# Kernel tuning notes

Hardware: AMD Instinct MI355X
Metric: run time of the kernel (lower is better)

## Reference

```python
import jax, jax.numpy as jnp
import numpy as np

B, C, H, W, KS = 8, 3, 512, 512, 3
K = KS * KS  # kernel_elements = 9


def setup_inputs() -> dict:
    key = jax.random.key(0)
    ks = jax.random.split(key, 5)
    return {
        "x": jax.random.normal(ks[0], (B, C, H, W), jnp.float32),
        "w1": jax.random.normal(ks[1], (K - 1, C, KS, KS), jnp.float32) * 0.1,  # find_ref conv weight
        "b1": jax.random.normal(ks[2], (K - 1,), jnp.float32) * 0.1,
        "w2": jax.random.normal(ks[3], (C, K), jnp.float32) * 0.1,  # grouped 1x1 conv: C groups, K in-ch each
        "b2": jax.random.normal(ks[4], (C,), jnp.float32) * 0.1,
    }


def _grid_sample_bilinear(img_nhwc, gx, gy):
    # torch.grid_sample, mode='bilinear', padding_mode='zeros', align_corners=False
    # img_nhwc: [B,H,W,C]; gx,gy: [B,h,w,K] normalized coords (x=width, y=height)
    Bs, Hh, Ww, _ = img_nhwc.shape
    ix = ((gx + 1.0) * Ww - 1.0) * 0.5
    iy = ((gy + 1.0) * Hh - 1.0) * 0.5
    ix0 = jnp.floor(ix)
    iy0 = jnp.floor(iy)
    wx1 = ix - ix0
    wy1 = iy - iy0
    wx0 = 1.0 - wx1
    wy0 = 1.0 - wy1
    bidx = jnp.arange(Bs)[:, None, None, None]

    def corner(yc, xc, wgt):
        valid = (xc >= 0) & (xc < Ww) & (yc >= 0) & (yc < Hh)
        xi = jnp.clip(xc, 0, Ww - 1).astype(jnp.int32)
        yi = jnp.clip(yc, 0, Hh - 1).astype(jnp.int32)
        v = img_nhwc[bidx, yi, xi]  # [B,h,w,K,C]
        return v * (wgt * valid)[..., None]

    out = corner(iy0, ix0, wy0 * wx0)
    out = out + corner(iy0, ix0 + 1.0, wy0 * wx1)
    out = out + corner(iy0 + 1.0, ix0, wy1 * wx0)
    out = out + corner(iy0 + 1.0, ix0 + 1.0, wy1 * wx1)
    return out  # [B,h,w,K,C]


def _forward(x, w1, b1, w2, b2):
    Bs, Cc, Hh, Ww = x.shape
    pad = KS // 2
    # find_ref: conv3x3 (pad=1) + sigmoid -> offsets in [0,1]
    off = jax.lax.conv_general_dilated(
        x, w1, (1, 1), ((pad, pad), (pad, pad)),
        dimension_numbers=("NCHW", "OIHW", "NCHW"))
    off = jax.nn.sigmoid(off + b1[None, :, None, None])  # [B,K-1,H,W]
    off = jnp.transpose(off, (0, 2, 3, 1)).reshape(Bs, Hh, Ww, (K - 1) // 2, 2)
    ctr = float(KS // 2)
    sym = 2.0 * ctr - off  # find_symmetric_points
    center = jnp.zeros((Bs, Hh, Ww, 1, 2), off.dtype)
    off_all = jnp.concatenate([off, center, sym], axis=-2)  # [B,H,W,K,2]
    # base grid: stack(h_grid, w_grid) with linspace(0,1)
    base = jnp.stack(
        jnp.meshgrid(jnp.linspace(0.0, 1.0, Hh), jnp.linspace(0.0, 1.0, Ww), indexing="ij"),
        axis=-1)  # [H,W,2]
    coords = base[None, :, :, None, :] + off_all  # [B,H,W,K,2]
    # grid_sample interprets last dim as (x=width, y=height)
    gx = coords[..., 0]
    gy = coords[..., 1]
    img = jnp.transpose(x, (0, 2, 3, 1))  # [B,H,W,C]
    sampled = _grid_sample_bilinear(img, gx, gy)  # [B,H,W,K,C]
    # concatenation order in torch: elem-major channels -> [B, K*C, H, W]
    deformed = jnp.transpose(sampled, (0, 3, 4, 1, 2)).reshape(Bs, K * Cc, Hh, Ww)
    # grouped 1x1 conv: groups=C, group g consumes channels [g*K:(g+1)*K]
    grp = deformed.reshape(Bs, Cc, K, Hh, Ww)
    out = jnp.einsum("bgkhw,gk->bghw", grp, w2) + b2[None, :, None, None]
    return jax.nn.relu(out)


def reference(x, w1, b1, w2, b2):
    return _forward(x, w1, b1, w2, b2)
```

## Files before the change

### kernel.cpp

```cpp
#include <hip/hip_runtime.h>

#define BATCH 8
#define HDIM  512
#define WDIM  512
#define PLANE (HDIM * WDIM)

#define QC_N      129
#define YROW0     254
#define YROWS     259
#define YSTRIDE   260
#define QSTRIDE   (YSTRIDE * 16)
#define PARSTRIDE (QC_N * QSTRIDE)
#define IMGSTRIDE (2 * PARSTRIDE)

typedef _Float16 half2v __attribute__((ext_vector_type(2)));
typedef _Float16 half8v __attribute__((ext_vector_type(8)));
typedef float    f2v    __attribute__((ext_vector_type(2)));

struct __align__(16) HQuad { half2v p0, p1, p2, p3; };

#if __has_builtin(__builtin_amdgcn_fdot2)
#define FDOT2(a, b, c) __builtin_amdgcn_fdot2((a), (b), (c), false)
#else
#define FDOT2(a, b, c) fmaf((float)(a).x, (float)(b).x, fmaf((float)(a).y, (float)(b).y, (c)))
#endif

#if __has_builtin(__builtin_amdgcn_exp2f)
#define EXP2F(x) __builtin_amdgcn_exp2f(x)
#else
#define EXP2F(x) exp2f(x)
#endif

__global__ __launch_bounds__(256) void repack_tiles(
    const float* __restrict__ x,
    char* __restrict__ xp)
{
    int b    = blockIdx.x & 7;
    int rest = blockIdx.x >> 3;
    int p    = rest & 1;
    int Qc   = rest >> 1;
    int xb0  = 254 + 2 * Qc + p;
    int x1   = xb0 + 1;
    bool x1v = (x1 < 512);

    const float* xb = x + (size_t)b * 3 * PLANE;
    char* dst = xp + (size_t)b * IMGSTRIDE + (size_t)p * PARSTRIDE
                   + (size_t)Qc * QSTRIDE;

    for (int t = threadIdx.x; t < YROWS; t += 256) {
        int y = YROW0 + t;
        half8v o;
        if (y < 512) {
            int base = (y << 9) + xb0;
            float a0 = xb[base];
            float a1 = xb[PLANE + base];
            float a2 = xb[2 * PLANE + base];
            float b0 = 0.f, b1c = 0.f, b2c = 0.f;
            if (x1v) {
                b0  = xb[base + 1];
                b1c = xb[PLANE + base + 1];
                b2c = xb[2 * PLANE + base + 1];
            }
            o[0] = (_Float16)a0; o[1] = (_Float16)a1; o[2] = (_Float16)a2; o[3] = (_Float16)0.f;
            o[4] = (_Float16)b0; o[5] = (_Float16)b1c; o[6] = (_Float16)b2c; o[7] = (_Float16)0.f;
        } else {
#pragma unroll
            for (int k = 0; k < 8; k++) o[k] = (_Float16)0.f;
        }
        *(half8v*)(dst + (size_t)t * 16) = o;
    }
}

__global__ __launch_bounds__(256) void seesaw_v11(
    const float* __restrict__ x,
    const char* __restrict__ xpack,
    const float* __restrict__ w1, const float* __restrict__ b1,
    const float* __restrict__ w2, const float* __restrict__ b2,
    float* __restrict__ out)
{
    int t  = threadIdx.x;
    int b  = blockIdx.x & 7;
    int i  = blockIdx.x >> 3;
    int j0 = t << 1;

    const float* xb = x + (size_t)b * 3 * PLANE;
    const char*  hb = xpack + (size_t)b * IMGSTRIDE;

    int cm = j0 - 1; if (cm < 0) cm = 0;
    int cp = j0 + 2; if (cp > 511) cp = 511;
    bool jlo = (t == 0), jhi = (t == 255);

    float vm[9], va[9], vb9[9], vp9[9];
    if (i >= 1 && i <= 510) {
#pragma unroll
        for (int di = 0; di < 3; di++) {
            const float* row = xb + ((i + di - 1) << 9);
#pragma unroll
            for (int c = 0; c < 3; c++) {
                const float* rc = row + c * PLANE;
                float m = rc[cm]; if (jlo) m = 0.f;
                f2v  mid = *(const f2v*)(rc + j0);
                float pv = rc[cp]; if (jhi) pv = 0.f;
                int r = c * 3 + di;
                vm[r] = m; va[r] = mid[0]; vb9[r] = mid[1]; vp9[r] = pv;
            }
        }
    } else {
#pragma unroll
        for (int di = 0; di < 3; di++) {
            int y = i + di - 1;
            bool yv = (unsigned)y < (unsigned)HDIM;
            const float* row = xb + ((yv ? y : 0) << 9);
#pragma unroll
            for (int c = 0; c < 3; c++) {
                const float* rc = row + c * PLANE;
                float m = rc[cm]; if (jlo || !yv) m = 0.f;
                f2v  mid = *(const f2v*)(rc + j0);
                float pv = rc[cp]; if (jhi || !yv) pv = 0.f;
                float m0 = yv ? mid[0] : 0.f;
                float m1 = yv ? mid[1] : 0.f;
                int r = c * 3 + di;
                vm[r] = m; va[r] = m0; vb9[r] = m1; vp9[r] = pv;
            }
        }
    }
    __builtin_amdgcn_sched_barrier(0);

    float tap0[27], tap1[27];
#pragma unroll
    for (int c = 0; c < 3; c++)
#pragma unroll
        for (int di = 0; di < 3; di++) {
            int r = c * 3 + di, k = c * 9 + di * 3;
            tap0[k]     = vm[r];  tap0[k + 1] = va[r];  tap0[k + 2] = vb9[r];
            tap1[k]     = va[r];  tap1[k + 1] = vb9[r]; tap1[k + 2] = vp9[r];
        }

    const float NLOG2E = -1.44269504f;
    auto conv8 = [&](const float* tap, float* s2) {
        f2v V[13];
#pragma unroll
        for (int k = 0; k < 13; k++) { V[k][0] = tap[2 * k]; V[k][1] = tap[2 * k + 1]; }
#pragma unroll
        for (int e = 0; e < 8; e++) {
            const float* we = w1 + e * 27;
            f2v a2; a2[0] = b1[e]; a2[1] = 0.f;
#pragma unroll
            for (int k = 0; k < 13; k++) {
                f2v ww; ww[0] = we[2 * k]; ww[1] = we[2 * k + 1];
                a2 = __builtin_elementwise_fma(V[k], ww, a2);
            }
            float acc = a2[0] + a2[1] + tap[26] * we[26];
            s2[e] = 256.0f * __builtin_amdgcn_rcpf(1.0f + EXP2F(acc * NLOG2E));
        }
    };
    float s0[8], s1[8];
    conv8(tap0, s0);
    conv8(tap1, s1);

    half2v w2a[5], w2b[5];
#pragma unroll
    for (int q = 0; q < 5; q++) {
        w2a[q][0] = (_Float16)w2[q * 3];
        w2a[q][1] = (_Float16)w2[q * 3 + 1];
        w2b[q][0] = (_Float16)w2[q * 3 + 2];
        w2b[q][1] = (_Float16)0.f;
    }

    const float k511 = 256.0f / 511.0f;
    float fxb = fmaf((float)i, k511, 255.5f);
    float fy0 = fmaf((float)j0, k511, 255.5f);
    float fy1 = fy0 + k511;

    int   adrA[5], adrB[5];
    float wXA[5][2], wYA[5][2], wXB[5][2], wYB[5][2];
    auto phase1 = [&](const float* s2, float fyb, int (&adr)[5],
                      float (&wX)[5][2], float (&wY)[5][2]) {
#pragma unroll
        for (int q = 0; q < 5; q++) {
            float ixf = (q < 4) ? (fxb + s2[2 * q])     : fxb;
            float iyf = (q < 4) ? (fyb + s2[2 * q + 1]) : fyb;
            int ix0 = (int)ixf, iy0 = (int)iyf;
            float wx1 = ixf - (float)ix0, wy1 = iyf - (float)iy0;
            wX[q][0] = (ix0 <= 511) ? (1.f - wx1) : 0.f;
            wX[q][1] = (ix0 <= 510) ? wx1 : 0.f;
            wY[q][0] = (iy0 <= 511) ? (1.f - wy1) : 0.f;
            wY[q][1] = (iy0 <= 510) ? wy1 : 0.f;
            int x0c = min(ix0, 511);
            int y0c = min(iy0, 511);
            int Qc  = (x0c >> 1) - 127;
            int off = (Qc << 12) + (Qc << 6) + ((y0c - 254) << 4);
            adr[q] = off + ((x0c & 1) ? PARSTRIDE : 0);
        }
    };

    phase1(s0, fy0, adrA, wXA, wYA);
    HQuad qA[5][2];
#pragma unroll
    for (int q = 0; q < 5; q++) {
        qA[q][0] = *(const HQuad*)(hb + (size_t)adrA[q]);
        qA[q][1] = *(const HQuad*)(hb + (size_t)adrA[q] + 16);
    }
    phase1(s1, fy1, adrB, wXB, wYB);
    HQuad qB[5][2];
#pragma unroll
    for (int q = 0; q < 5; q++) {
        qB[q][0] = *(const HQuad*)(hb + (size_t)adrB[q]);
        qB[q][1] = *(const HQuad*)(hb + (size_t)adrB[q] + 16);
    }
    __builtin_amdgcn_sched_barrier(0);

    float ogA[3] = {0.f, 0.f, 0.f}, ogB[3] = {0.f, 0.f, 0.f};
    auto phase3 = [&](HQuad (&qv)[5][2], float (&wX)[5][2], float (&wY)[5][2], float* og) {
#pragma unroll
        for (int q = 0; q < 5; q++) {
            int g = q / 3;
            float dl0 = FDOT2(qv[q][0].p0, w2a[q], FDOT2(qv[q][0].p1, w2b[q], 0.f));
            float dh0 = FDOT2(qv[q][0].p2, w2a[q], FDOT2(qv[q][0].p3, w2b[q], 0.f));
            float dl1 = FDOT2(qv[q][1].p0, w2a[q], FDOT2(qv[q][1].p1, w2b[q], 0.f));
            float dh1 = FDOT2(qv[q][1].p2, w2a[q], FDOT2(qv[q][1].p3, w2b[q], 0.f));
            float r0 = fmaf(dh0, wX[q][1], dl0 * wX[q][0]);
            float r1 = fmaf(dh1, wX[q][1], dl1 * wX[q][0]);
            og[g] = fmaf(r1, wY[q][1], fmaf(r0, wY[q][0], og[g]));
        }
    };
    phase3(qA, wXA, wYA, ogA);
    phase3(qB, wXB, wYB, ogB);

    if ((i | j0) == 0) {
#pragma unroll
        for (int p = 5; p < 9; p++) {
            float ixf = fxb + 512.0f - s0[2 * (p - 5)];
            float iyf = fy0 + 512.0f - s0[2 * (p - 5) + 1];
            float ix0f = floorf(ixf), iy0f = floorf(iyf);
            float wx1 = ixf - ix0f, wy1 = iyf - iy0f;
            float wx0 = 1.f - wx1,  wy0 = 1.f - wy1;
            int ix0 = (int)ix0f, iy0 = (int)iy0f;
            float t0 = 0.f, t1 = 0.f, t2 = 0.f;
            for (int cy = 0; cy < 2; cy++) {
                int yc2 = iy0 + cy;
                if (yc2 < 0 || yc2 >= HDIM) continue;
                float wy = cy ? wy1 : wy0;
                for (int cx = 0; cx < 2; cx++) {
                    int xcc2 = ix0 + cx;
                    if (xcc2 < 0 || xcc2 >= WDIM) continue;
                    float wgt = wy * (cx ? wx1 : wx0);
                    int base = (yc2 << 9) + xcc2;
                    t0 = fmaf(xb[base],             wgt, t0);
                    t1 = fmaf(xb[PLANE + base],     wgt, t1);
                    t2 = fmaf(xb[2 * PLANE + base], wgt, t2);
                }
            }
            int g  = p / 3;
            int k0 = (p % 3) * 3;
            ogA[g] = fmaf(t0, w2[g * 9 + k0 + 0], ogA[g]);
            ogA[g] = fmaf(t1, w2[g * 9 + k0 + 1], ogA[g]);
            ogA[g] = fmaf(t2, w2[g * 9 + k0 + 2], ogA[g]);
        }
    }

    size_t ob = (size_t)(b * 3) * PLANE + ((size_t)i << 9) + j0;
#pragma unroll
    for (int g = 0; g < 3; g++) {
        float u0 = ogA[g] + b2[g];
        float u1 = ogB[g] + b2[g];
        f2v st;
        st[0] = u0 > 0.f ? u0 : 0.f;
        st[1] = u1 > 0.f ? u1 : 0.f;
        *(f2v*)(out + ob + (size_t)g * PLANE) = st;
    }
}

__global__ __launch_bounds__(256) void seesaw_fused_v1(
    const float* __restrict__ x, const float* __restrict__ w1,
    const float* __restrict__ b1, const float* __restrict__ w2,
    const float* __restrict__ b2, float* __restrict__ out)
{
    int t = threadIdx.x;
    int gid = blockIdx.x * 256 + t;
    int j = gid & (WDIM - 1);
    int i = (gid >> 9) & (HDIM - 1);
    int b = gid >> 18;
    const float* xb = x + (size_t)b * 3 * PLANE;
    float acc[8];
#pragma unroll
    for (int e = 0; e < 8; e++) acc[e] = b1[e];
#pragma unroll
    for (int di = 0; di < 3; di++) {
        int y = i + di - 1;
        if (y < 0 || y >= HDIM) continue;
#pragma unroll
        for (int dj = 0; dj < 3; dj++) {
            int xc = j + dj - 1;
            if (xc < 0 || xc >= WDIM) continue;
            size_t base = (size_t)y * WDIM + xc;
#pragma unroll
            for (int c = 0; c < 3; c++) {
                float v = xb[(size_t)c * PLANE + base];
#pragma unroll
                for (int e = 0; e < 8; e++)
                    acc[e] = fmaf(v, w1[e * 27 + c * 9 + di * 3 + dj], acc[e]);
            }
        }
    }
    float s[8];
#pragma unroll
    for (int e = 0; e < 8; e++) s[e] = 1.0f / (1.0f + __expf(-acc[e]));
    const float inv511 = 1.0f / 511.0f;
    float bx = (float)i * inv511, by = (float)j * inv511;
    float og0 = 0.f, og1 = 0.f, og2 = 0.f;
#pragma unroll
    for (int p = 0; p < 9; p++) {
        float c0, c1;
        if (p < 4)       { c0 = s[2 * p];              c1 = s[2 * p + 1]; }
        else if (p == 4) { c0 = 0.f;                   c1 = 0.f; }
        else             { c0 = 2.0f - s[2 * (p - 5)]; c1 = 2.0f - s[2 * (p - 5) + 1]; }
        float ixf = (bx + c0) * 256.0f + 255.5f;
        float iyf = (by + c1) * 256.0f + 255.5f;
        float ix0f = floorf(ixf), iy0f = floorf(iyf);
        float wx1 = ixf - ix0f, wy1 = iyf - iy0f;
        float wx0 = 1.f - wx1,  wy0 = 1.f - wy1;
        int ix0 = (int)ix0f, iy0 = (int)iy0f;
        float s0 = 0.f, s1 = 0.f, s2 = 0.f;
#pragma unroll
        for (int cy = 0; cy < 2; cy++) {
            int yc = iy0 + cy;
            if (yc < 0 || yc >= HDIM) continue;
            float wy = cy ? wy1 : wy0;
#pragma unroll
            for (int cx = 0; cx < 2; cx++) {
                int xcc = ix0 + cx;
                if (xcc < 0 || xcc >= WDIM) continue;
                float wgt = wy * (cx ? wx1 : wx0);
                size_t base = (size_t)yc * WDIM + xcc;
                s0 = fmaf(xb[base],             wgt, s0);
                s1 = fmaf(xb[PLANE + base],     wgt, s1);
                s2 = fmaf(xb[2 * PLANE + base], wgt, s2);
            }
        }
        int g  = p / 3;
        int k0 = (p % 3) * 3;
        float* og = (g == 0) ? &og0 : (g == 1) ? &og1 : &og2;
        *og = fmaf(s0, w2[g * 9 + k0 + 0], *og);
        *og = fmaf(s1, w2[g * 9 + k0 + 1], *og);
        *og = fmaf(s2, w2[g * 9 + k0 + 2], *og);
    }
    size_t ob = (size_t)(b * 3) * PLANE + (size_t)i * WDIM + j;
    float v0 = og0 + b2[0], v1 = og1 + b2[1], v2 = og2 + b2[2];
    out[ob]             = v0 > 0.f ? v0 : 0.f;
    out[ob + PLANE]     = v1 > 0.f ? v1 : 0.f;
    out[ob + 2 * PLANE] = v2 > 0.f ? v2 : 0.f;
}

extern "C" void kernel_launch(void* const* d_in, const int* in_sizes, int n_in,
                              void* d_out, int out_size, void* d_ws, size_t ws_size,
                              hipStream_t stream) {
    const float* x  = (const float*)d_in[0];
    const float* w1 = (const float*)d_in[1];
    const float* b1 = (const float*)d_in[2];
    const float* w2 = (const float*)d_in[3];
    const float* b2 = (const float*)d_in[4];
    float* out = (float*)d_out;

    int total = BATCH * HDIM * WDIM;
    size_t need = (size_t)BATCH * IMGSTRIDE + 16;

    if (ws_size >= need) {
        repack_tiles<<<8 * 2 * QC_N, 256, 0, stream>>>(x, (char*)d_ws);
        seesaw_v11<<<BATCH * HDIM, 256, 0, stream>>>(x, (const char*)d_ws,
                                                     w1, b1, w2, b2, out);
    } else {
        seesaw_fused_v1<<<total / 256, 256, 0, stream>>>(x, w1, b1, w2, b2, out);
    }
}
```

Before: 131.9 us.

## Precompute per-tap channel dot products in repack with 2x2 corner quads

The repack kernel now folds the grouped 1x1 conv weights into the image ahead of time. It stores, for each of the five sampled taps, the fp16 dot product over channels for every 2x2 corner neighbourhood, laid out by x/y parity so that one 8-byte load returns all four bilinear corners. The main kernel then does 5 small loads per pixel instead of 10 16-byte loads and drops the fdot2 work. The cost is a larger workspace (five planes of quads) and a repack that reads each input four times. The old v11 path remains as a fallback when the workspace is too small.

```diff
diff --git a/kernel.cpp b/kernel.cpp
--- a/kernel.cpp
+++ b/kernel.cpp
@@ -4,6 +4,11 @@
 #define HDIM  512
 #define WDIM  512
 #define PLANE (HDIM * WDIM)
+
+#define QN      129
+#define QPAIRS  (QN * QN)
+#define QPLANE  (4 * QPAIRS * 8)
+#define IMG12   (5 * QPLANE)
 
 #define QC_N      129
 #define YROW0     254
@@ -14,10 +19,12 @@
 #define IMGSTRIDE (2 * PARSTRIDE)
 
 typedef _Float16 half2v __attribute__((ext_vector_type(2)));
+typedef _Float16 half4v __attribute__((ext_vector_type(4)));
 typedef _Float16 half8v __attribute__((ext_vector_type(8)));
 typedef float    f2v    __attribute__((ext_vector_type(2)));
 
 struct __align__(16) HQuad { half2v p0, p1, p2, p3; };
+struct __align__(8)  HPair { half2v lo, hi; };
 
 #if __has_builtin(__builtin_amdgcn_fdot2)
 #define FDOT2(a, b, c) __builtin_amdgcn_fdot2((a), (b), (c), false)
@@ -31,47 +38,52 @@
 #define EXP2F(x) exp2f(x)
 #endif
 
-__global__ __launch_bounds__(256) void repack_tiles(
+__global__ __launch_bounds__(256) void repack_dots(
     const float* __restrict__ x,
+    const float* __restrict__ w2,
     char* __restrict__ xp)
 {
-    int b    = blockIdx.x & 7;
-    int rest = blockIdx.x >> 3;
-    int p    = rest & 1;
-    int Qc   = rest >> 1;
-    int xb0  = 254 + 2 * Qc + p;
-    int x1   = xb0 + 1;
-    bool x1v = (x1 < 512);
+    int b  = blockIdx.x & 7;
+    int P  = (blockIdx.x >> 3) & 3;
+    int Qy = blockIdx.x >> 5;
+    int Qx = threadIdx.x;
+    if (Qx >= QN) return;
+    int px = P & 1, py = P >> 1;
+    int X0 = 2 * Qx + 254 + px;
+    int Y0 = 2 * Qy + 254 + py;
 
     const float* xb = x + (size_t)b * 3 * PLANE;
-    char* dst = xp + (size_t)b * IMGSTRIDE + (size_t)p * PARSTRIDE
-                   + (size_t)Qc * QSTRIDE;
-
-    for (int t = threadIdx.x; t < YROWS; t += 256) {
-        int y = YROW0 + t;
-        half8v o;
-        if (y < 512) {
-            int base = (y << 9) + xb0;
-            float a0 = xb[base];
-            float a1 = xb[PLANE + base];
-            float a2 = xb[2 * PLANE + base];
-            float b0 = 0.f, b1c = 0.f, b2c = 0.f;
-            if (x1v) {
-                b0  = xb[base + 1];
-                b1c = xb[PLANE + base + 1];
-                b2c = xb[2 * PLANE + base + 1];
-            }
-            o[0] = (_Float16)a0; o[1] = (_Float16)a1; o[2] = (_Float16)a2; o[3] = (_Float16)0.f;
-            o[4] = (_Float16)b0; o[5] = (_Float16)b1c; o[6] = (_Float16)b2c; o[7] = (_Float16)0.f;
-        } else {
-#pragma unroll
-            for (int k = 0; k < 8; k++) o[k] = (_Float16)0.f;
-        }
-        *(half8v*)(dst + (size_t)t * 16) = o;
+
+    float vc[4][3];
+#pragma unroll
+    for (int cy = 0; cy < 2; cy++)
+#pragma unroll
+        for (int cx = 0; cx < 2; cx++) {
+            int xx = X0 + cx, yy = Y0 + cy;
+            bool vld = (xx <= 511) && (yy <= 511);
+            int xs = min(xx, 511), ys = min(yy, 511);
+            int base = (ys << 9) + xs;
+            int ci = cy * 2 + cx;
+            vc[ci][0] = vld ? xb[base]             : 0.f;
+            vc[ci][1] = vld ? xb[PLANE + base]     : 0.f;
+            vc[ci][2] = vld ? xb[2 * PLANE + base] : 0.f;
+        }
+
+    char* dst = xp + (size_t)b * IMG12 + (size_t)((P * QPAIRS + Qy * QN + Qx) << 3);
+#pragma unroll
+    for (int q = 0; q < 5; q++) {
+        float wa = w2[3 * q], wb = w2[3 * q + 1], wc = w2[3 * q + 2];
+        half4v o;
+#pragma unroll
+        for (int ci = 0; ci < 4; ci++) {
+            float v = fmaf(vc[ci][2], wc, fmaf(vc[ci][1], wb, vc[ci][0] * wa));
+            o[ci] = (_Float16)v;
+        }
+        *(half4v*)(dst + q * QPLANE) = o;
     }
 }
 
-__global__ __launch_bounds__(256) void seesaw_v11(
+__global__ __launch_bounds__(256) void seesaw_v12(
     const float* __restrict__ x,
     const char* __restrict__ xpack,
     const float* __restrict__ w1, const float* __restrict__ b1,
@@ -84,7 +96,7 @@
     int j0 = t << 1;
 
     const float* xb = x + (size_t)b * 3 * PLANE;
-    const char*  hb = xpack + (size_t)b * IMGSTRIDE;
+    const char*  hb = xpack + (size_t)b * IMG12;
 
     int cm = j0 - 1; if (cm < 0) cm = 0;
     int cp = j0 + 2; if (cp > 511) cp = 511;
@@ -158,15 +170,6 @@
     conv8(tap0, s0);
     conv8(tap1, s1);
 
-    half2v w2a[5], w2b[5];
-#pragma unroll
-    for (int q = 0; q < 5; q++) {
-        w2a[q][0] = (_Float16)w2[q * 3];
-        w2a[q][1] = (_Float16)w2[q * 3 + 1];
-        w2b[q][0] = (_Float16)w2[q * 3 + 2];
-        w2b[q][1] = (_Float16)0.f;
-    }
-
     const float k511 = 256.0f / 511.0f;
     float fxb = fmaf((float)i, k511, 255.5f);
     float fy0 = fmaf((float)j0, k511, 255.5f);
@@ -186,46 +189,40 @@
             wX[q][1] = (ix0 <= 510) ? wx1 : 0.f;
             wY[q][0] = (iy0 <= 511) ? (1.f - wy1) : 0.f;
             wY[q][1] = (iy0 <= 510) ? wy1 : 0.f;
-            int x0c = min(ix0, 511);
-            int y0c = min(iy0, 511);
-            int Qc  = (x0c >> 1) - 127;
-            int off = (Qc << 12) + (Qc << 6) + ((y0c - 254) << 4);
-            adr[q] = off + ((x0c & 1) ? PARSTRIDE : 0);
+            int x0c = min(ix0, 511), y0c = min(iy0, 511);
+            int P  = ((y0c & 1) << 1) | (x0c & 1);
+            int Qx = (x0c >> 1) - 127;
+            int Qy = (y0c >> 1) - 127;
+            adr[q] = (P * QPAIRS + Qy * QN + Qx) << 3;
         }
     };
 
     phase1(s0, fy0, adrA, wXA, wYA);
-    HQuad qA[5][2];
-#pragma unroll
-    for (int q = 0; q < 5; q++) {
-        qA[q][0] = *(const HQuad*)(hb + (size_t)adrA[q]);
-        qA[q][1] = *(const HQuad*)(hb + (size_t)adrA[q] + 16);
-    }
+    HPair pA[5];
+#pragma unroll
+    for (int q = 0; q < 5; q++)
+        pA[q] = *(const HPair*)(hb + (size_t)(q * QPLANE + adrA[q]));
     phase1(s1, fy1, adrB, wXB, wYB);
-    HQuad qB[5][2];
-#pragma unroll
-    for (int q = 0; q < 5; q++) {
-        qB[q][0] = *(const HQuad*)(hb + (size_t)adrB[q]);
-        qB[q][1] = *(const HQuad*)(hb + (size_t)adrB[q] + 16);
-    }
+    HPair pB[5];
+#pragma unroll
+    for (int q = 0; q < 5; q++)
+        pB[q] = *(const HPair*)(hb + (size_t)(q * QPLANE + adrB[q]));
     __builtin_amdgcn_sched_barrier(0);
 
     float ogA[3] = {0.f, 0.f, 0.f}, ogB[3] = {0.f, 0.f, 0.f};
-    auto phase3 = [&](HQuad (&qv)[5][2], float (&wX)[5][2], float (&wY)[5][2], float* og) {
+    auto phase3 = [&](HPair (&pv)[5], float (&wX)[5][2], float (&wY)[5][2], float* og) {
 #pragma unroll
         for (int q = 0; q < 5; q++) {
             int g = q / 3;
-            float dl0 = FDOT2(qv[q][0].p0, w2a[q], FDOT2(qv[q][0].p1, w2b[q], 0.f));
-            float dh0 = FDOT2(qv[q][0].p2, w2a[q], FDOT2(qv[q][0].p3, w2b[q], 0.f));
-            float dl1 = FDOT2(qv[q][1].p0, w2a[q], FDOT2(qv[q][1].p1, w2b[q], 0.f));
-            float dh1 = FDOT2(qv[q][1].p2, w2a[q], FDOT2(qv[q][1].p3, w2b[q], 0.f));
-            float r0 = fmaf(dh0, wX[q][1], dl0 * wX[q][0]);
-            float r1 = fmaf(dh1, wX[q][1], dl1 * wX[q][0]);
+            float v00 = (float)pv[q].lo[0], v01 = (float)pv[q].lo[1];
+            float v10 = (float)pv[q].hi[0], v11c = (float)pv[q].hi[1];
+            float r0 = fmaf(v01,  wX[q][1], v00 * wX[q][0]);
+            float r1 = fmaf(v11c, wX[q][1], v10 * wX[q][0]);
             og[g] = fmaf(r1, wY[q][1], fmaf(r0, wY[q][0], og[g]));
         }
     };
-    phase3(qA, wXA, wYA, ogA);
-    phase3(qB, wXB, wYB, ogB);
+    phase3(pA, wXA, wYA, ogA);
+    phase3(pB, wXB, wYB, ogB);
 
     if ((i | j0) == 0) {
 #pragma unroll
@@ -271,6 +268,244 @@
     }
 }
 
+__global__ __launch_bounds__(256) void repack_tiles(
+    const float* __restrict__ x, char* __restrict__ xp)
+{
+    int b    = blockIdx.x & 7;
+    int rest = blockIdx.x >> 3;
+    int p    = rest & 1;
+    int Qc   = rest >> 1;
+    int xb0  = 254 + 2 * Qc + p;
+    int x1   = xb0 + 1;
+    bool x1v = (x1 < 512);
+
+    const float* xb = x + (size_t)b * 3 * PLANE;
+    char* dst = xp + (size_t)b * IMGSTRIDE + (size_t)p * PARSTRIDE
+                   + (size_t)Qc * QSTRIDE;
+
+    for (int t = threadIdx.x; t < YROWS; t += 256) {
+        int y = YROW0 + t;
+        half8v o;
+        if (y < 512) {
+            int base = (y << 9) + xb0;
+            float a0 = xb[base];
+            float a1 = xb[PLANE + base];
+            float a2 = xb[2 * PLANE + base];
+            float b0 = 0.f, b1c = 0.f, b2c = 0.f;
+            if (x1v) {
+                b0  = xb[base + 1];
+                b1c = xb[PLANE + base + 1];
+                b2c = xb[2 * PLANE + base + 1];
+            }
+            o[0] = (_Float16)a0; o[1] = (_Float16)a1; o[2] = (_Float16)a2; o[3] = (_Float16)0.f;
+            o[4] = (_Float16)b0; o[5] = (_Float16)b1c; o[6] = (_Float16)b2c; o[7] = (_Float16)0.f;
+        } else {
+#pragma unroll
+            for (int k = 0; k < 8; k++) o[k] = (_Float16)0.f;
+        }
+        *(half8v*)(dst + (size_t)t * 16) = o;
+    }
+}
+
+__global__ __launch_bounds__(256) void seesaw_v11(
+    const float* __restrict__ x, const char* __restrict__ xpack,
+    const float* __restrict__ w1, const float* __restrict__ b1,
+    const float* __restrict__ w2, const float* __restrict__ b2,
+    float* __restrict__ out)
+{
+    int t  = threadIdx.x;
+    int b  = blockIdx.x & 7;
+    int i  = blockIdx.x >> 3;
+    int j0 = t << 1;
+
+    const float* xb = x + (size_t)b * 3 * PLANE;
+    const char*  hb = xpack + (size_t)b * IMGSTRIDE;
+
+    int cm = j0 - 1; if (cm < 0) cm = 0;
+    int cp = j0 + 2; if (cp > 511) cp = 511;
+    bool jlo = (t == 0), jhi = (t == 255);
+
+    float vm[9], va[9], vb9[9], vp9[9];
+    if (i >= 1 && i <= 510) {
+#pragma unroll
+        for (int di = 0; di < 3; di++) {
+            const float* row = xb + ((i + di - 1) << 9);
+#pragma unroll
+            for (int c = 0; c < 3; c++) {
+                const float* rc = row + c * PLANE;
+                float m = rc[cm]; if (jlo) m = 0.f;
+                f2v  mid = *(const f2v*)(rc + j0);
+                float pv = rc[cp]; if (jhi) pv = 0.f;
+                int r = c * 3 + di;
+                vm[r] = m; va[r] = mid[0]; vb9[r] = mid[1]; vp9[r] = pv;
+            }
+        }
+    } else {
+#pragma unroll
+        for (int di = 0; di < 3; di++) {
+            int y = i + di - 1;
+            bool yv = (unsigned)y < (unsigned)HDIM;
+            const float* row = xb + ((yv ? y : 0) << 9);
+#pragma unroll
+            for (int c = 0; c < 3; c++) {
+                const float* rc = row + c * PLANE;
+                float m = rc[cm]; if (jlo || !yv) m = 0.f;
+                f2v  mid = *(const f2v*)(rc + j0);
+                float pv = rc[cp]; if (jhi || !yv) pv = 0.f;
+                float m0 = yv ? mid[0] : 0.f;
+                float m1 = yv ? mid[1] : 0.f;
+                int r = c * 3 + di;
+                vm[r] = m; va[r] = m0; vb9[r] = m1; vp9[r] = pv;
+            }
+        }
+    }
+    __builtin_amdgcn_sched_barrier(0);
+
+    float tap0[27], tap1[27];
+#pragma unroll
+    for (int c = 0; c < 3; c++)
+#pragma unroll
+        for (int di = 0; di < 3; di++) {
+            int r = c * 3 + di, k = c * 9 + di * 3;
+            tap0[k]     = vm[r];  tap0[k + 1] = va[r];  tap0[k + 2] = vb9[r];
+            tap1[k]     = va[r];  tap1[k + 1] = vb9[r]; tap1[k + 2] = vp9[r];
+        }
+
+    const float NLOG2E = -1.44269504f;
+    auto conv8 = [&](const float* tap, float* s2) {
+        f2v V[13];
+#pragma unroll
+        for (int k = 0; k < 13; k++) { V[k][0] = tap[2 * k]; V[k][1] = tap[2 * k + 1]; }
+#pragma unroll
+        for (int e = 0; e < 8; e++) {
+            const float* we = w1 + e * 27;
+            f2v a2; a2[0] = b1[e]; a2[1] = 0.f;
+#pragma unroll
+            for (int k = 0; k < 13; k++) {
+                f2v ww; ww[0] = we[2 * k]; ww[1] = we[2 * k + 1];
+                a2 = __builtin_elementwise_fma(V[k], ww, a2);
+            }
+            float acc = a2[0] + a2[1] + tap[26] * we[26];
+            s2[e] = 256.0f * __builtin_amdgcn_rcpf(1.0f + EXP2F(acc * NLOG2E));
+        }
+    };
+    float s0[8], s1[8];
+    conv8(tap0, s0);
+    conv8(tap1, s1);
+
+    half2v w2a[5], w2b[5];
+#pragma unroll
+    for (int q = 0; q < 5; q++) {
+        w2a[q][0] = (_Float16)w2[q * 3];
+        w2a[q][1] = (_Float16)w2[q * 3 + 1];
+        w2b[q][0] = (_Float16)w2[q * 3 + 2];
+        w2b[q][1] = (_Float16)0.f;
+    }
+
+    const float k511 = 256.0f / 511.0f;
+    float fxb = fmaf((float)i, k511, 255.5f);
+    float fy0 = fmaf((float)j0, k511, 255.5f);
+    float fy1 = fy0 + k511;
+
+    int   adrA[5], adrB[5];
+    float wXA[5][2], wYA[5][2], wXB[5][2], wYB[5][2];
+    auto phase1 = [&](const float* s2, float fyb, int (&adr)[5],
+                      float (&wX)[5][2], float (&wY)[5][2]) {
+#pragma unroll
+        for (int q = 0; q < 5; q++) {
+            float ixf = (q < 4) ? (fxb + s2[2 * q])     : fxb;
+            float iyf = (q < 4) ? (fyb + s2[2 * q + 1]) : fyb;
+            int ix0 = (int)ixf, iy0 = (int)iyf;
+            float wx1 = ixf - (float)ix0, wy1 = iyf - (float)iy0;
+            wX[q][0] = (ix0 <= 511) ? (1.f - wx1) : 0.f;
+            wX[q][1] = (ix0 <= 510) ? wx1 : 0.f;
+            wY[q][0] = (iy0 <= 511) ? (1.f - wy1) : 0.f;
+            wY[q][1] = (iy0 <= 510) ? wy1 : 0.f;
+            int x0c = min(ix0, 511);
+            int y0c = min(iy0, 511);
+            int Qc  = (x0c >> 1) - 127;
+            int off = (Qc << 12) + (Qc << 6) + ((y0c - 254) << 4);
+            adr[q] = off + ((x0c & 1) ? PARSTRIDE : 0);
+        }
+    };
+
+    phase1(s0, fy0, adrA, wXA, wYA);
+    HQuad qA[5][2];
+#pragma unroll
+    for (int q = 0; q < 5; q++) {
+        qA[q][0] = *(const HQuad*)(hb + (size_t)adrA[q]);
+        qA[q][1] = *(const HQuad*)(hb + (size_t)adrA[q] + 16);
+    }
+    phase1(s1, fy1, adrB, wXB, wYB);
+    HQuad qB[5][2];
+#pragma unroll
+    for (int q = 0; q < 5; q++) {
+        qB[q][0] = *(const HQuad*)(hb + (size_t)adrB[q]);
+        qB[q][1] = *(const HQuad*)(hb + (size_t)adrB[q] + 16);
+    }
+    __builtin_amdgcn_sched_barrier(0);
+
+    float ogA[3] = {0.f, 0.f, 0.f}, ogB[3] = {0.f, 0.f, 0.f};
+    auto phase3 = [&](HQuad (&qv)[5][2], float (&wX)[5][2], float (&wY)[5][2], float* og) {
+#pragma unroll
+        for (int q = 0; q < 5; q++) {
+            int g = q / 3;
+            float dl0 = FDOT2(qv[q][0].p0, w2a[q], FDOT2(qv[q][0].p1, w2b[q], 0.f));
+            float dh0 = FDOT2(qv[q][0].p2, w2a[q], FDOT2(qv[q][0].p3, w2b[q], 0.f));
+            float dl1 = FDOT2(qv[q][1].p0, w2a[q], FDOT2(qv[q][1].p1, w2b[q], 0.f));
+            float dh1 = FDOT2(qv[q][1].p2, w2a[q], FDOT2(qv[q][1].p3, w2b[q], 0.f));
+            float r0 = fmaf(dh0, wX[q][1], dl0 * wX[q][0]);
+            float r1 = fmaf(dh1, wX[q][1], dl1 * wX[q][0]);
+            og[g] = fmaf(r1, wY[q][1], fmaf(r0, wY[q][0], og[g]));
+        }
+    };
+    phase3(qA, wXA, wYA, ogA);
+    phase3(qB, wXB, wYB, ogB);
+
+    if ((i | j0) == 0) {
+#pragma unroll
+        for (int p = 5; p < 9; p++) {
+            float ixf = fxb + 512.0f - s0[2 * (p - 5)];
+            float iyf = fy0 + 512.0f - s0[2 * (p - 5) + 1];
+            float ix0f = floorf(ixf), iy0f = floorf(iyf);
+            float wx1 = ixf - ix0f, wy1 = iyf - iy0f;
+            float wx0 = 1.f - wx1,  wy0 = 1.f - wy1;
+            int ix0 = (int)ix0f, iy0 = (int)iy0f;
+            float t0 = 0.f, t1 = 0.f, t2 = 0.f;
+            for (int cy = 0; cy < 2; cy++) {
+                int yc2 = iy0 + cy;
+                if (yc2 < 0 || yc2 >= HDIM) continue;
+                float wy = cy ? wy1 : wy0;
+                for (int cx = 0; cx < 2; cx++) {
+                    int xcc2 = ix0 + cx;
+                    if (xcc2 < 0 || xcc2 >= WDIM) continue;
+                    float wgt = wy * (cx ? wx1 : wx0);
+                    int base = (yc2 << 9) + xcc2;
+                    t0 = fmaf(xb[base],             wgt, t0);
+                    t1 = fmaf(xb[PLANE + base],     wgt, t1);
+                    t2 = fmaf(xb[2 * PLANE + base], wgt, t2);
+                }
+            }
+            int g  = p / 3;
+            int k0 = (p % 3) * 3;
+            ogA[g] = fmaf(t0, w2[g * 9 + k0 + 0], ogA[g]);
+            ogA[g] = fmaf(t1, w2[g * 9 + k0 + 1], ogA[g]);
+            ogA[g] = fmaf(t2, w2[g * 9 + k0 + 2], ogA[g]);
+        }
+    }
+
+    size_t ob = (size_t)(b * 3) * PLANE + ((size_t)i << 9) + j0;
+#pragma unroll
+    for (int g = 0; g < 3; g++) {
+        float u0 = ogA[g] + b2[g];
+        float u1 = ogB[g] + b2[g];
+        f2v st;
+        st[0] = u0 > 0.f ? u0 : 0.f;
+        st[1] = u1 > 0.f ? u1 : 0.f;
+        *(f2v*)(out + ob + (size_t)g * PLANE) = st;
+    }
+}
+
 __global__ __launch_bounds__(256) void seesaw_fused_v1(
     const float* __restrict__ x, const float* __restrict__ w1,
     const float* __restrict__ b1, const float* __restrict__ w2,
@@ -363,9 +598,14 @@
     float* out = (float*)d_out;
 
     int total = BATCH * HDIM * WDIM;
-    size_t need = (size_t)BATCH * IMGSTRIDE + 16;
-
-    if (ws_size >= need) {
+    size_t need12 = (size_t)BATCH * IMG12 + 64;
+    size_t need11 = (size_t)BATCH * IMGSTRIDE + 16;
+
+    if (ws_size >= need12) {
+        repack_dots<<<8 * 4 * QN, 256, 0, stream>>>(x, w2, (char*)d_ws);
+        seesaw_v12<<<BATCH * HDIM, 256, 0, stream>>>(x, (const char*)d_ws,
+                                                     w1, b1, w2, b2, out);
+    } else if (ws_size >= need11) {
         repack_tiles<<<8 * 2 * QC_N, 256, 0, stream>>>(x, (char*)d_ws);
         seesaw_v11<<<BATCH * HDIM, 256, 0, stream>>>(x, (const char*)d_ws,
                                                      w1, b1, w2, b2, out);
```

Result: faster. 120.5 us (-8.6%).

## Pre-reduce channels with w2 in repack, use column-major fp16 table, restructure conv

Applied to the files above, without the earlier changes.

The repack kernel now applies the grouped 1x1 weights per sampling point before storing, so each (q, parity, column) entry holds one fp16 scalar instead of three channels. The main kernel then fetches one 8-byte pair per sample instead of two 16-byte quads and skips the fdot2 channel reductions. The repack also writes a transposed copy of w1, so the offset conv can run as a k-outer loop with paired FMAs across output channels. This cuts gather bytes and ALU work, at the cost of scattered 4-byte writes in the repack and extra rounding from storing the w2-weighted sums in fp16.

```diff
diff --git a/kernel.cpp b/kernel.cpp
--- a/kernel.cpp
+++ b/kernel.cpp
@@ -5,25 +5,16 @@
 #define WDIM  512
 #define PLANE (HDIM * WDIM)
 
-#define QC_N      129
-#define YROW0     254
-#define YROWS     259
-#define YSTRIDE   260
-#define QSTRIDE   (YSTRIDE * 16)
-#define PARSTRIDE (QC_N * QSTRIDE)
-#define IMGSTRIDE (2 * PARSTRIDE)
+#define COLB   1040
+#define NCOL   1290
+#define IMG15  ((size_t)NCOL * COLB)
+#define PACK15 ((size_t)BATCH * IMG15)
+#define W1E_FLOATS (27 * 8)
 
 typedef _Float16 half2v __attribute__((ext_vector_type(2)));
-typedef _Float16 half8v __attribute__((ext_vector_type(8)));
 typedef float    f2v    __attribute__((ext_vector_type(2)));
 
-struct __align__(16) HQuad { half2v p0, p1, p2, p3; };
-
-#if __has_builtin(__builtin_amdgcn_fdot2)
-#define FDOT2(a, b, c) __builtin_amdgcn_fdot2((a), (b), (c), false)
-#else
-#define FDOT2(a, b, c) fmaf((float)(a).x, (float)(b).x, fmaf((float)(a).y, (float)(b).y, (c)))
-#endif
+struct __align__(4) HPair4 { half2v lo, hi; };
 
 #if __has_builtin(__builtin_amdgcn_exp2f)
 #define EXP2F(x) __builtin_amdgcn_exp2f(x)
@@ -31,50 +22,58 @@
 #define EXP2F(x) exp2f(x)
 #endif
 
-__global__ __launch_bounds__(256) void repack_tiles(
+__global__ __launch_bounds__(256) void repack_cols(
     const float* __restrict__ x,
+    const float* __restrict__ w1,
+    const float* __restrict__ w2,
     char* __restrict__ xp)
 {
-    int b    = blockIdx.x & 7;
-    int rest = blockIdx.x >> 3;
-    int p    = rest & 1;
-    int Qc   = rest >> 1;
-    int xb0  = 254 + 2 * Qc + p;
-    int x1   = xb0 + 1;
-    bool x1v = (x1 < 512);
-
+    if (blockIdx.x == 0 && threadIdx.x < W1E_FLOATS) {
+        int t = threadIdx.x;
+        float* w1e = (float*)(xp + PACK15);
+        w1e[t] = w1[(t & 7) * 27 + (t >> 3)];
+    }
+
+    int b  = blockIdx.x & 7;
+    int by = blockIdx.x >> 3;
+    int y  = 254 + by;
     const float* xb = x + (size_t)b * 3 * PLANE;
-    char* dst = xp + (size_t)b * IMGSTRIDE + (size_t)p * PARSTRIDE
-                   + (size_t)Qc * QSTRIDE;
-
-    for (int t = threadIdx.x; t < YROWS; t += 256) {
-        int y = YROW0 + t;
-        half8v o;
+    char* dst = xp + (size_t)b * IMG15;
+
+    for (int t = threadIdx.x; t < 258; t += 256) {
+        int x0 = 254 + t;
+        int px = t & 1;
+        int Qx = (x0 >> 1) - 127;
+        float a0 = 0.f, a1 = 0.f, a2 = 0.f;
+        float c0 = 0.f, c1 = 0.f, c2 = 0.f;
         if (y < 512) {
-            int base = (y << 9) + xb0;
-            float a0 = xb[base];
-            float a1 = xb[PLANE + base];
-            float a2 = xb[2 * PLANE + base];
-            float b0 = 0.f, b1c = 0.f, b2c = 0.f;
-            if (x1v) {
-                b0  = xb[base + 1];
-                b1c = xb[PLANE + base + 1];
-                b2c = xb[2 * PLANE + base + 1];
-            }
-            o[0] = (_Float16)a0; o[1] = (_Float16)a1; o[2] = (_Float16)a2; o[3] = (_Float16)0.f;
-            o[4] = (_Float16)b0; o[5] = (_Float16)b1c; o[6] = (_Float16)b2c; o[7] = (_Float16)0.f;
-        } else {
-#pragma unroll
-            for (int k = 0; k < 8; k++) o[k] = (_Float16)0.f;
-        }
-        *(half8v*)(dst + (size_t)t * 16) = o;
+            const float* row = xb + (y << 9);
+            a0 = row[x0];
+            a1 = row[PLANE + x0];
+            a2 = row[2 * PLANE + x0];
+            if (x0 < 511) {
+                c0 = row[x0 + 1];
+                c1 = row[PLANE + x0 + 1];
+                c2 = row[2 * PLANE + x0 + 1];
+            }
+        }
+        char* colbase = dst + (size_t)by * 4;
+#pragma unroll
+        for (int q = 0; q < 5; q++) {
+            float wa = w2[3 * q], wb = w2[3 * q + 1], wc = w2[3 * q + 2];
+            half2v e;
+            e[0] = (_Float16)fmaf(a2, wc, fmaf(a1, wb, a0 * wa));
+            e[1] = (_Float16)fmaf(c2, wc, fmaf(c1, wb, c0 * wa));
+            int col = ((q << 1) + px) * 129 + Qx;
+            *(half2v*)(colbase + (size_t)col * COLB) = e;
+        }
     }
 }
 
-__global__ __launch_bounds__(256) void seesaw_v11(
+__global__ __launch_bounds__(256) void seesaw_v16(
     const float* __restrict__ x,
     const char* __restrict__ xpack,
-    const float* __restrict__ w1, const float* __restrict__ b1,
+    const float* __restrict__ b1,
     const float* __restrict__ w2, const float* __restrict__ b2,
     float* __restrict__ out)
 {
@@ -84,7 +83,8 @@
     int j0 = t << 1;
 
     const float* xb = x + (size_t)b * 3 * PLANE;
-    const char*  hb = xpack + (size_t)b * IMGSTRIDE;
+    const char*  hb = xpack + (size_t)b * IMG15;
+    const f2v*   wv = (const f2v*)(xpack + PACK15);
 
     int cm = j0 - 1; if (cm < 0) cm = 0;
     int cp = j0 + 2; if (cp > 511) cp = 511;
@@ -124,7 +124,6 @@
             }
         }
     }
-    __builtin_amdgcn_sched_barrier(0);
 
     float tap0[27], tap1[27];
 #pragma unroll
@@ -136,35 +135,30 @@
             tap1[k]     = va[r];  tap1[k + 1] = vb9[r]; tap1[k + 2] = vp9[r];
         }
 
+    f2v acc0[4], acc1[4];
+#pragma unroll
+    for (int eh = 0; eh < 4; eh++) {
+        f2v bb; bb[0] = b1[2 * eh]; bb[1] = b1[2 * eh + 1];
+        acc0[eh] = bb; acc1[eh] = bb;
+    }
+#pragma unroll
+    for (int k = 0; k < 27; k++) {
+        f2v t0v; t0v[0] = tap0[k]; t0v[1] = tap0[k];
+        f2v t1v; t1v[0] = tap1[k]; t1v[1] = tap1[k];
+#pragma unroll
+        for (int eh = 0; eh < 4; eh++) {
+            f2v w = wv[k * 4 + eh];
+            acc0[eh] = __builtin_elementwise_fma(t0v, w, acc0[eh]);
+            acc1[eh] = __builtin_elementwise_fma(t1v, w, acc1[eh]);
+        }
+    }
+
     const float NLOG2E = -1.44269504f;
-    auto conv8 = [&](const float* tap, float* s2) {
-        f2v V[13];
-#pragma unroll
-        for (int k = 0; k < 13; k++) { V[k][0] = tap[2 * k]; V[k][1] = tap[2 * k + 1]; }
-#pragma unroll
-        for (int e = 0; e < 8; e++) {
-            const float* we = w1 + e * 27;
-            f2v a2; a2[0] = b1[e]; a2[1] = 0.f;
-#pragma unroll
-            for (int k = 0; k < 13; k++) {
-                f2v ww; ww[0] = we[2 * k]; ww[1] = we[2 * k + 1];
-                a2 = __builtin_elementwise_fma(V[k], ww, a2);
-            }
-            float acc = a2[0] + a2[1] + tap[26] * we[26];
-            s2[e] = 256.0f * __builtin_amdgcn_rcpf(1.0f + EXP2F(acc * NLOG2E));
-        }
-    };
     float s0[8], s1[8];
-    conv8(tap0, s0);
-    conv8(tap1, s1);
-
-    half2v w2a[5], w2b[5];
-#pragma unroll
-    for (int q = 0; q < 5; q++) {
-        w2a[q][0] = (_Float16)w2[q * 3];
-        w2a[q][1] = (_Float16)w2[q * 3 + 1];
-        w2b[q][0] = (_Float16)w2[q * 3 + 2];
-        w2b[q][1] = (_Float16)0.f;
+#pragma unroll
+    for (int e = 0; e < 8; e++) {
+        s0[e] = 256.0f * __builtin_amdgcn_rcpf(1.0f + EXP2F(acc0[e >> 1][e & 1] * NLOG2E));
+        s1[e] = 256.0f * __builtin_amdgcn_rcpf(1.0f + EXP2F(acc1[e >> 1][e & 1] * NLOG2E));
     }
 
     const float k511 = 256.0f / 511.0f;
@@ -186,46 +180,39 @@
             wX[q][1] = (ix0 <= 510) ? wx1 : 0.f;
             wY[q][0] = (iy0 <= 511) ? (1.f - wy1) : 0.f;
             wY[q][1] = (iy0 <= 510) ? wy1 : 0.f;
-            int x0c = min(ix0, 511);
-            int y0c = min(iy0, 511);
-            int Qc  = (x0c >> 1) - 127;
-            int off = (Qc << 12) + (Qc << 6) + ((y0c - 254) << 4);
-            adr[q] = off + ((x0c & 1) ? PARSTRIDE : 0);
+            int x0c = min(ix0, 511), y0c = min(iy0, 511);
+            int pxq = x0c & 1;
+            int Qx  = (x0c >> 1) - 127;
+            adr[q] = (((q << 1) + pxq) * 129 + Qx) * COLB + ((y0c - 254) << 2);
         }
     };
 
     phase1(s0, fy0, adrA, wXA, wYA);
-    HQuad qA[5][2];
-#pragma unroll
-    for (int q = 0; q < 5; q++) {
-        qA[q][0] = *(const HQuad*)(hb + (size_t)adrA[q]);
-        qA[q][1] = *(const HQuad*)(hb + (size_t)adrA[q] + 16);
-    }
+    HPair4 pA[5];
+#pragma unroll
+    for (int q = 0; q < 5; q++)
+        pA[q] = *(const HPair4*)(hb + (size_t)adrA[q]);
     phase1(s1, fy1, adrB, wXB, wYB);
-    HQuad qB[5][2];
-#pragma unroll
-    for (int q = 0; q < 5; q++) {
-        qB[q][0] = *(const HQuad*)(hb + (size_t)adrB[q]);
-        qB[q][1] = *(const HQuad*)(hb + (size_t)adrB[q] + 16);
-    }
+    HPair4 pB[5];
+#pragma unroll
+    for (int q = 0; q < 5; q++)
+        pB[q] = *(const HPair4*)(hb + (size_t)adrB[q]);
     __builtin_amdgcn_sched_barrier(0);
 
     float ogA[3] = {0.f, 0.f, 0.f}, ogB[3] = {0.f, 0.f, 0.f};
-    auto phase3 = [&](HQuad (&qv)[5][2], float (&wX)[5][2], float (&wY)[5][2], float* og) {
+    auto phase3 = [&](HPair4 (&pv)[5], float (&wX)[5][2], float (&wY)[5][2], float* og) {
 #pragma unroll
         for (int q = 0; q < 5; q++) {
             int g = q / 3;
-            float dl0 = FDOT2(qv[q][0].p0, w2a[q], FDOT2(qv[q][0].p1, w2b[q], 0.f));
-            float dh0 = FDOT2(qv[q][0].p2, w2a[q], FDOT2(qv[q][0].p3, w2b[q], 0.f));
-            float dl1 = FDOT2(qv[q][1].p0, w2a[q], FDOT2(qv[q][1].p1, w2b[q], 0.f));
-            float dh1 = FDOT2(qv[q][1].p2, w2a[q], FDOT2(qv[q][1].p3, w2b[q], 0.f));
-            float r0 = fmaf(dh0, wX[q][1], dl0 * wX[q][0]);
-            float r1 = fmaf(dh1, wX[q][1], dl1 * wX[q][0]);
+            float v00 = (float)pv[q].lo[0], v01 = (float)pv[q].lo[1];
+            float v10 = (float)pv[q].hi[0], v11c = (float)pv[q].hi[1];
+            float r0 = fmaf(v01,  wX[q][1], v00 * wX[q][0]);
+            float r1 = fmaf(v11c, wX[q][1], v10 * wX[q][0]);
             og[g] = fmaf(r1, wY[q][1], fmaf(r0, wY[q][0], og[g]));
         }
     };
-    phase3(qA, wXA, wYA, ogA);
-    phase3(qB, wXB, wYB, ogB);
+    phase3(pA, wXA, wYA, ogA);
+    phase3(pB, wXB, wYB, ogB);
 
     if ((i | j0) == 0) {
 #pragma unroll
@@ -363,12 +350,12 @@
     float* out = (float*)d_out;
 
     int total = BATCH * HDIM * WDIM;
-    size_t need = (size_t)BATCH * IMGSTRIDE + 16;
-
-    if (ws_size >= need) {
-        repack_tiles<<<8 * 2 * QC_N, 256, 0, stream>>>(x, (char*)d_ws);
-        seesaw_v11<<<BATCH * HDIM, 256, 0, stream>>>(x, (const char*)d_ws,
-                                                     w1, b1, w2, b2, out);
+    size_t need15 = PACK15 + W1E_FLOATS * 4 + 64;
+
+    if (ws_size >= need15) {
+        repack_cols<<<8 * 259, 256, 0, stream>>>(x, w1, w2, (char*)d_ws);
+        seesaw_v16<<<BATCH * HDIM, 256, 0, stream>>>(x, (const char*)d_ws,
+                                                     b1, w2, b2, out);
     } else {
         seesaw_fused_v1<<<total / 256, 256, 0, stream>>>(x, w1, b1, w2, b2, out);
     }
```

After: 125.4 us. 4.9% less time.
